# Kernel tuning notes

Measured on AMD Instinct MI355X. Metric: run time of the kernel, lower is better.

The kernel has to match this reference:

```python
import jax, jax.numpy as jnp
import numpy as np

K = 16  # number of nearest neighbors


def setup_inputs() -> dict:
    key = jax.random.key(0)
    k1, k2, k3 = jax.random.split(key, 3)
    B, N, C, C_OUT = 2, 8192, 64, 64
    coords_knn = jax.random.normal(k1, (B, N, 3), dtype=jnp.float32)
    feat = jax.random.normal(k2, (B, N, C), dtype=jnp.float32)
    # MLP params: Linear(2*C + 3 -> C_OUT)
    W = jax.random.normal(k3, (2 * C + 3, C_OUT), dtype=jnp.float32) * 0.05
    b = jnp.zeros((C_OUT,), dtype=jnp.float32)
    return {"coords_knn": coords_knn, "feat": feat, "W": W, "b": b}


def _knn_idx(coords, k):
    # pairwise squared distances: ||xi||^2 + ||xj||^2 - 2 xi.xj   -> [B, N, N]
    xx = jnp.sum(coords ** 2, axis=-1, keepdims=True)
    dist = xx + jnp.swapaxes(xx, 1, 2) - 2.0 * jnp.einsum('bnc,bmc->bnm', coords, coords)
    dist = jnp.maximum(dist, 0.0)
    _, idx = jax.lax.top_k(-dist, k)  # k smallest distances (order irrelevant: max-pool)
    return idx  # [B, N, k] int32


def reference(coords_knn, feat, W, b):
    idx = _knn_idx(coords_knn, K)
    gather = jax.vmap(lambda a, i: a[i])          # per-batch gather: [N,C],[N,k] -> [N,k,C]
    nb_f = gather(feat, idx)                      # [B, N, k, C]
    nb_p = gather(coords_knn, idx)                # [B, N, k, 3]
    fi = feat[:, :, None, :]                      # [B, N, 1, C]
    pi = coords_knn[:, :, None, :]                # [B, N, 1, 3]
    x = jnp.concatenate(
        [jnp.broadcast_to(fi, nb_f.shape), nb_f - fi, nb_p - pi], axis=-1
    )                                             # [B, N, k, 2C+3]
    x = jax.nn.relu(jnp.einsum('bnkd,do->bnko', x, W) + b)
    return jnp.max(x, axis=2)                     # [B, N, C_OUT]
```

## Files before the change

kernel.cpp:

```cpp
#include <hip/hip_runtime.h>
#include <hip/hip_bf16.h>
#include <stdint.h>
#include <float.h>

#define B_ 2
#define N_ 8192
#define C_ 64
#define K_ 16
#define D_IN 131
#define QPB 16
#define QPW 4
#define CAP 192
#define SAMPLE_N 2048

typedef __attribute__((ext_vector_type(8))) short short8v;
typedef __attribute__((ext_vector_type(4))) float f32x4;
typedef unsigned long long ull;

#define SENT_U64 0x7F7FFFFFFFFFFFFFull

__device__ __forceinline__ float sq3(float x, float y, float z) {
#pragma clang fp contract(off)
  return (x * x + y * y) + z * z;
}

__device__ __forceinline__ uint64_t shfl_xor_u64(uint64_t x, int mask) {
  int lo = __shfl_xor((int)(uint32_t)(x & 0xffffffffull), mask, 64);
  int hi = __shfl_xor((int)(uint32_t)(x >> 32), mask, 64);
  return ((uint64_t)(uint32_t)hi << 32) | (uint32_t)lo;
}

__device__ __forceinline__ double shfl_xor_f64(double x, int mask) {
  return __builtin_bit_cast(double, shfl_xor_u64(__builtin_bit_cast(uint64_t, x), mask));
}

__device__ __forceinline__ uint64_t pack_key_u64(float d, int idx) {
  return ((uint64_t)__float_as_uint(d) << 32) | (uint32_t)idx;
}

__device__ __forceinline__ short bfs(float x) {
  return __builtin_bit_cast(short, __float2bfloat16(x));
}

__device__ __forceinline__ void insert16(double* hd, double key) {
  hd[15] = key;
#pragma unroll
  for (int z = 15; z >= 1; --z) {
    double a = hd[z - 1], b = hd[z];
    hd[z - 1] = fmin(a, b);
    hd[z] = fmax(a, b);
  }
}

__device__ __forceinline__ float exact_d(float qx, float qy, float qz, float xxq,
                                         float4 cd) {
  float dot2 = fmaf(qz, cd.z, fmaf(qy, cd.y, qx * cd.x));
  float dtmp;
  {
#pragma clang fp contract(off)
    dtmp = (xxq + cd.w) - dot2;
  }
  return fmaxf(dtmp, 0.0f);
}

__global__ __launch_bounds__(256) void prep(const float* __restrict__ coords,
                                            const float* __restrict__ W,
                                            __hip_bfloat16* __restrict__ wfrag,
                                            float4* __restrict__ c4) {
  int i = blockIdx.x * 256 + threadIdx.x;
  if (i < 4 * 5 * 64 * 8) {
    int j = i & 7;
    int l = (i >> 3) & 63;
    int ks = (i >> 9) % 5;
    int nt = (i >> 9) / 5;
    int k = ks * 32 + (l >> 4) * 8 + j;
    int col = nt * 16 + (l & 15);
    float v = (k < D_IN) ? W[k * 64 + col] : 0.0f;
    wfrag[i] = __float2bfloat16(v);
  }
  int j2 = i - 4 * 5 * 64 * 8;
  if (j2 >= 0 && j2 < B_ * N_) {
    float cx = coords[j2 * 3 + 0], cy = coords[j2 * 3 + 1], cz = coords[j2 * 3 + 2];
    c4[j2] = make_float4(2.0f * cx, 2.0f * cy, 2.0f * cz, sq3(cx, cy, cz));
  }
}

__global__ __launch_bounds__(256) void knn_kernel(const float* __restrict__ coords,
                                                  const float4* __restrict__ c4,
                                                  int* __restrict__ idxout) {
  __shared__ int sbuf[QPB][CAP];
  __shared__ int scnt[QPB];
  const int t = threadIdx.x;
  const int w = t >> 6;
  const int lane = t & 63;
  const int blk = blockIdx.x;
  const int bb = blk >> 9;
  const int qbase = (blk & 511) * QPB;
  const float* cb = coords + (size_t)bb * N_ * 3;
  const float4* cg = c4 + (size_t)bb * N_;

  float qx[QPW], qy[QPW], qz[QPW], xxq[QPW];
#pragma unroll
  for (int r = 0; r < QPW; ++r) {
    int n = qbase + w * QPW + r;
    qx[r] = cb[n * 3 + 0]; qy[r] = cb[n * 3 + 1]; qz[r] = cb[n * 3 + 2];
    xxq[r] = sq3(qx[r], qy[r], qz[r]);
  }
  if (t < QPB) scnt[t] = 0;
  __syncthreads();

#define PROXY(r, cd) fmaf(qz[r], (cd).z, fmaf(qy[r], (cd).y, fmaf(qx[r], (cd).x, -(cd).w)))

  float M1[QPW], M2[QPW];
#pragma unroll
  for (int r = 0; r < QPW; ++r) { M1[r] = -FLT_MAX; M2[r] = -FLT_MAX; }

  for (int j0 = 0; j0 < SAMPLE_N; j0 += 512) {
    float4 c0 = cg[j0 + lane];
    float4 c1 = cg[j0 + 64 + lane];
    float4 c2 = cg[j0 + 128 + lane];
    float4 c3 = cg[j0 + 192 + lane];
    float4 c4v = cg[j0 + 256 + lane];
    float4 c5 = cg[j0 + 320 + lane];
    float4 c6 = cg[j0 + 384 + lane];
    float4 c7 = cg[j0 + 448 + lane];
#pragma unroll
    for (int r = 0; r < QPW; ++r) {
      float p0 = PROXY(r, c0);
      float p1 = PROXY(r, c1);
      float p2 = PROXY(r, c2);
      float p3 = PROXY(r, c3);
      float p4 = PROXY(r, c4v);
      float p5 = PROXY(r, c5);
      float p6 = PROXY(r, c6);
      float p7 = PROXY(r, c7);
      float a1 = fmaxf(p0, p1), b1 = fminf(p0, p1);
      float a2 = fmaxf(p2, p3), b2 = fminf(p2, p3);
      float a3 = fmaxf(p4, p5), b3 = fminf(p4, p5);
      float a4 = fmaxf(p6, p7), b4 = fminf(p6, p7);
      float h12 = fmaxf(a1, a2), s12 = fmaxf(fminf(a1, a2), fmaxf(b1, b2));
      float h34 = fmaxf(a3, a4), s34 = fmaxf(fminf(a3, a4), fmaxf(b3, b4));
      float hi = fmaxf(h12, h34);
      float se = fmaxf(fminf(h12, h34), fmaxf(s12, s34));
      float nm2 = fmaxf(fminf(M1[r], hi), fmaxf(M2[r], se));
      M1[r] = fmaxf(M1[r], hi);
      M2[r] = nm2;
    }
  }

  float A[QPW], Bt[QPW], pT[QPW];
#pragma unroll
  for (int r = 0; r < QPW; ++r) { A[r] = M1[r]; Bt[r] = M2[r]; pT[r] = -FLT_MAX; }
#pragma unroll
  for (int rd = 0; rd < 16; ++rd) {
#pragma unroll
    for (int r = 0; r < QPW; ++r) {
      float g = fmaxf(A[r], Bt[r]);
      g = fmaxf(g, __shfl_xor(g, 1, 64));
      g = fmaxf(g, __shfl_xor(g, 2, 64));
      g = fmaxf(g, __shfl_xor(g, 4, 64));
      g = fmaxf(g, __shfl_xor(g, 8, 64));
      g = fmaxf(g, __shfl_xor(g, 16, 64));
      g = fmaxf(g, __shfl_xor(g, 32, 64));
      pT[r] = g;
      A[r] = (A[r] == g) ? -FLT_MAX : A[r];
      Bt[r] = (Bt[r] == g) ? -FLT_MAX : Bt[r];
    }
  }
  float X[QPW];
#pragma unroll
  for (int r = 0; r < QPW; ++r) {
    float slop = 6e-6f * (fabsf(xxq[r]) + fabsf(pT[r])) + 1e-5f;
    X[r] = fminf(pT[r], xxq[r]) - 2.0f * slop;
  }

  for (int j0 = 0; j0 < N_; j0 += 512) {
    const int ia = j0 + lane;
    float4 c0 = cg[ia];
    float4 c1 = cg[ia + 64];
    float4 c2 = cg[ia + 128];
    float4 c3 = cg[ia + 192];
    float4 c4v = cg[ia + 256];
    float4 c5 = cg[ia + 320];
    float4 c6 = cg[ia + 384];
    float4 c7 = cg[ia + 448];
#pragma unroll
    for (int r = 0; r < QPW; ++r) {
      float p0 = PROXY(r, c0);
      float p1 = PROXY(r, c1);
      float p2 = PROXY(r, c2);
      float p3 = PROXY(r, c3);
      float p4 = PROXY(r, c4v);
      float p5 = PROXY(r, c5);
      float p6 = PROXY(r, c6);
      float p7 = PROXY(r, c7);
      const int qr = w * QPW + r;
      if (p0 >= X[r]) { int pos = atomicAdd(&scnt[qr], 1); if (pos < CAP) sbuf[qr][pos] = ia; }
      if (p1 >= X[r]) { int pos = atomicAdd(&scnt[qr], 1); if (pos < CAP) sbuf[qr][pos] = ia + 64; }
      if (p2 >= X[r]) { int pos = atomicAdd(&scnt[qr], 1); if (pos < CAP) sbuf[qr][pos] = ia + 128; }
      if (p3 >= X[r]) { int pos = atomicAdd(&scnt[qr], 1); if (pos < CAP) sbuf[qr][pos] = ia + 192; }
      if (p4 >= X[r]) { int pos = atomicAdd(&scnt[qr], 1); if (pos < CAP) sbuf[qr][pos] = ia + 256; }
      if (p5 >= X[r]) { int pos = atomicAdd(&scnt[qr], 1); if (pos < CAP) sbuf[qr][pos] = ia + 320; }
      if (p6 >= X[r]) { int pos = atomicAdd(&scnt[qr], 1); if (pos < CAP) sbuf[qr][pos] = ia + 384; }
      if (p7 >= X[r]) { int pos = atomicAdd(&scnt[qr], 1); if (pos < CAP) sbuf[qr][pos] = ia + 448; }
    }
  }
  __syncthreads();

  const int qloc = t >> 4;
  const int s16 = t & 15;
  const int n = qbase + qloc;

  const float fqx = cb[n * 3 + 0], fqy = cb[n * 3 + 1], fqz = cb[n * 3 + 2];
  const float fxx = sq3(fqx, fqy, fqz);

  double hd[16];
#pragma unroll
  for (int i = 0; i < 16; ++i) hd[i] = __builtin_bit_cast(double, SENT_U64);

  const int cntv = scnt[qloc];
  if (cntv > CAP) {
    for (int j = s16; j < N_; j += 16) {
      float cx = cb[j * 3 + 0], cy = cb[j * 3 + 1], cz = cb[j * 3 + 2];
      float ww = sq3(cx, cy, cz);
      float dot = fmaf(fqz, cz, fmaf(fqy, cy, fqx * cx));
      float d2;
      {
#pragma clang fp contract(off)
        d2 = (fxx + ww) - 2.0f * dot;
      }
      d2 = fmaxf(d2, 0.0f);
      double k = __builtin_bit_cast(double, pack_key_u64(d2, j));
      if (k < hd[15]) insert16(hd, k);
    }
  } else {
    for (int i = s16; i < cntv; i += 16) {
      int idx = sbuf[qloc][i];
      float d = exact_d(fqx, fqy, fqz, fxx, cg[idx]);
      double k = __builtin_bit_cast(double, pack_key_u64(d, idx));
      if (k < hd[15]) insert16(hd, k);
    }
  }

  int* myout = idxout + ((size_t)(bb * N_ + n)) * K_;
#pragma unroll
  for (int r = 0; r < 16; ++r) {
    double v = hd[0];
    v = fmin(v, shfl_xor_f64(v, 1));
    v = fmin(v, shfl_xor_f64(v, 2));
    v = fmin(v, shfl_xor_f64(v, 4));
    v = fmin(v, shfl_xor_f64(v, 8));
    if (__builtin_bit_cast(uint64_t, hd[0]) == __builtin_bit_cast(uint64_t, v)) {
#pragma unroll
      for (int z = 0; z < 15; ++z) hd[z] = hd[z + 1];
      hd[15] = __builtin_bit_cast(double, SENT_U64);
    }
    if (s16 == 0) myout[r] = (int)(uint32_t)__builtin_bit_cast(uint64_t, v);
  }
}

__global__ __launch_bounds__(256) void stage2(const float* __restrict__ coords,
                                              const float* __restrict__ feat,
                                              const int* __restrict__ idxbuf,
                                              const __hip_bfloat16* __restrict__ wfrag,
                                              const float* __restrict__ bias,
                                              float* __restrict__ out) {
  const int t = threadIdx.x;
  const int w = t >> 6;
  const int lane = t & 63;
  const int q = blockIdx.x * 4 + w;
  const int bb = q >> 13;
  const int n = q & (N_ - 1);
  const float* cb = coords + (size_t)bb * N_ * 3;
  const float* fb = feat + (size_t)bb * N_ * C_;
  const int* myidx = idxbuf + (size_t)q * K_;

  const int row = lane & 15;
  const int g = lane >> 4;
  const int nb = myidx[row];

  const float* fq = fb + (size_t)n * C_;
  const float* fn = fb + (size_t)nb * C_;

  float4 fi0 = *(const float4*)&fq[g * 8];
  float4 fi1 = *(const float4*)&fq[g * 8 + 4];
  float4 fi2 = *(const float4*)&fq[32 + g * 8];
  float4 fi3 = *(const float4*)&fq[32 + g * 8 + 4];
  float4 nf0 = *(const float4*)&fn[g * 8];
  float4 nf1 = *(const float4*)&fn[g * 8 + 4];
  float4 nf2 = *(const float4*)&fn[32 + g * 8];
  float4 nf3 = *(const float4*)&fn[32 + g * 8 + 4];

  short8v a[5];
  a[0] = (short8v){bfs(fi0.x), bfs(fi0.y), bfs(fi0.z), bfs(fi0.w),
                   bfs(fi1.x), bfs(fi1.y), bfs(fi1.z), bfs(fi1.w)};
  a[1] = (short8v){bfs(fi2.x), bfs(fi2.y), bfs(fi2.z), bfs(fi2.w),
                   bfs(fi3.x), bfs(fi3.y), bfs(fi3.z), bfs(fi3.w)};
  a[2] = (short8v){bfs(nf0.x - fi0.x), bfs(nf0.y - fi0.y), bfs(nf0.z - fi0.z), bfs(nf0.w - fi0.w),
                   bfs(nf1.x - fi1.x), bfs(nf1.y - fi1.y), bfs(nf1.z - fi1.z), bfs(nf1.w - fi1.w)};
  a[3] = (short8v){bfs(nf2.x - fi2.x), bfs(nf2.y - fi2.y), bfs(nf2.z - fi2.z), bfs(nf2.w - fi2.w),
                   bfs(nf3.x - fi3.x), bfs(nf3.y - fi3.y), bfs(nf3.z - fi3.z), bfs(nf3.w - fi3.w)};
  if (g == 0) {
    a[4] = (short8v){bfs(cb[nb * 3 + 0] - cb[n * 3 + 0]),
                     bfs(cb[nb * 3 + 1] - cb[n * 3 + 1]),
                     bfs(cb[nb * 3 + 2] - cb[n * 3 + 2]),
                     0, 0, 0, 0, 0};
  } else {
    a[4] = (short8v){0, 0, 0, 0, 0, 0, 0, 0};
  }

  const short8v* wf = (const short8v*)wfrag;
#pragma unroll
  for (int nt = 0; nt < 4; ++nt) {
    f32x4 acc = {0.f, 0.f, 0.f, 0.f};
#pragma unroll
    for (int ks = 0; ks < 5; ++ks) {
      short8v bf = wf[(nt * 5 + ks) * 64 + lane];
      acc = __builtin_amdgcn_mfma_f32_16x16x32_bf16(a[ks], bf, acc, 0, 0, 0);
    }
    float bcol = bias[nt * 16 + row];
    float m = fmaxf(fmaxf(fmaxf(acc[0] + bcol, 0.f), fmaxf(acc[1] + bcol, 0.f)),
                    fmaxf(fmaxf(acc[2] + bcol, 0.f), fmaxf(acc[3] + bcol, 0.f)));
    m = fmaxf(m, __shfl_xor(m, 16, 64));
    m = fmaxf(m, __shfl_xor(m, 32, 64));
    if (lane < 16) out[(size_t)q * C_ + nt * 16 + row] = m;
  }
}

extern "C" void kernel_launch(void* const* d_in, const int* in_sizes, int n_in,
                              void* d_out, int out_size, void* d_ws, size_t ws_size,
                              hipStream_t stream) {
  const float* coords = (const float*)d_in[0];
  const float* feat = (const float*)d_in[1];
  const float* W = (const float*)d_in[2];
  const float* bias = (const float*)d_in[3];
  float* out = (float*)d_out;

  int* ws_idx = (int*)d_ws;
  char* p = (char*)d_ws + (size_t)B_ * N_ * K_ * sizeof(int);
  __hip_bfloat16* wfrag = (__hip_bfloat16*)p;
  float4* c4 = (float4*)(p + 32768);

  const int prep_elems = 4 * 5 * 64 * 8 + B_ * N_;
  prep<<<(prep_elems + 255) / 256, 256, 0, stream>>>(coords, W, wfrag, c4);
  knn_kernel<<<(B_ * N_) / QPB, 256, 0, stream>>>(coords, c4, ws_idx);
  stage2<<<(B_ * N_) / 4, 256, 0, stream>>>(coords, feat, ws_idx, wfrag, bias, out);
}
```

Before: 91.13 us.

## Fuse KNN selection and MLP max-pool stage into one kernel

Merges the KNN kernel and the MFMA MLP stage into one kernel. Neighbor indices now stay in shared memory instead of going through a global workspace, and one kernel launch is removed. Each wave then runs the MLP for its 4 queries in sequence, so the MLP work is spread over far fewer blocks than the old stage2 grid. It also shares the KNN kernel's register and shared-memory footprint, which may lower occupancy for the gather and MFMA part.

```diff
diff --git a/kernel.cpp b/kernel.cpp
--- a/kernel.cpp
+++ b/kernel.cpp
@@ -85,11 +85,15 @@
   }
 }
 
-__global__ __launch_bounds__(256) void knn_kernel(const float* __restrict__ coords,
-                                                  const float4* __restrict__ c4,
-                                                  int* __restrict__ idxout) {
+__global__ __launch_bounds__(256) void knn_fused(const float* __restrict__ coords,
+                                                 const float4* __restrict__ c4,
+                                                 const float* __restrict__ feat,
+                                                 const __hip_bfloat16* __restrict__ wfrag,
+                                                 const float* __restrict__ bias,
+                                                 float* __restrict__ out) {
   __shared__ int sbuf[QPB][CAP];
   __shared__ int scnt[QPB];
+  __shared__ int sidx[QPB][K_];
   const int t = threadIdx.x;
   const int w = t >> 6;
   const int lane = t & 63;
@@ -242,7 +246,6 @@
     }
   }
 
-  int* myout = idxout + ((size_t)(bb * N_ + n)) * K_;
 #pragma unroll
   for (int r = 0; r < 16; ++r) {
     double v = hd[0];
@@ -255,75 +258,65 @@
       for (int z = 0; z < 15; ++z) hd[z] = hd[z + 1];
       hd[15] = __builtin_bit_cast(double, SENT_U64);
     }
-    if (s16 == 0) myout[r] = (int)(uint32_t)__builtin_bit_cast(uint64_t, v);
-  }
-}
-
-__global__ __launch_bounds__(256) void stage2(const float* __restrict__ coords,
-                                              const float* __restrict__ feat,
-                                              const int* __restrict__ idxbuf,
-                                              const __hip_bfloat16* __restrict__ wfrag,
-                                              const float* __restrict__ bias,
-                                              float* __restrict__ out) {
-  const int t = threadIdx.x;
-  const int w = t >> 6;
-  const int lane = t & 63;
-  const int q = blockIdx.x * 4 + w;
-  const int bb = q >> 13;
-  const int n = q & (N_ - 1);
-  const float* cb = coords + (size_t)bb * N_ * 3;
+    if (s16 == 0) sidx[qloc][r] = (int)(uint32_t)__builtin_bit_cast(uint64_t, v);
+  }
+  __syncthreads();
+
   const float* fb = feat + (size_t)bb * N_ * C_;
-  const int* myidx = idxbuf + (size_t)q * K_;
-
+  const short8v* wf = (const short8v*)wfrag;
   const int row = lane & 15;
   const int g = lane >> 4;
-  const int nb = myidx[row];
-
-  const float* fq = fb + (size_t)n * C_;
-  const float* fn = fb + (size_t)nb * C_;
-
-  float4 fi0 = *(const float4*)&fq[g * 8];
-  float4 fi1 = *(const float4*)&fq[g * 8 + 4];
-  float4 fi2 = *(const float4*)&fq[32 + g * 8];
-  float4 fi3 = *(const float4*)&fq[32 + g * 8 + 4];
-  float4 nf0 = *(const float4*)&fn[g * 8];
-  float4 nf1 = *(const float4*)&fn[g * 8 + 4];
-  float4 nf2 = *(const float4*)&fn[32 + g * 8];
-  float4 nf3 = *(const float4*)&fn[32 + g * 8 + 4];
-
-  short8v a[5];
-  a[0] = (short8v){bfs(fi0.x), bfs(fi0.y), bfs(fi0.z), bfs(fi0.w),
-                   bfs(fi1.x), bfs(fi1.y), bfs(fi1.z), bfs(fi1.w)};
-  a[1] = (short8v){bfs(fi2.x), bfs(fi2.y), bfs(fi2.z), bfs(fi2.w),
-                   bfs(fi3.x), bfs(fi3.y), bfs(fi3.z), bfs(fi3.w)};
-  a[2] = (short8v){bfs(nf0.x - fi0.x), bfs(nf0.y - fi0.y), bfs(nf0.z - fi0.z), bfs(nf0.w - fi0.w),
-                   bfs(nf1.x - fi1.x), bfs(nf1.y - fi1.y), bfs(nf1.z - fi1.z), bfs(nf1.w - fi1.w)};
-  a[3] = (short8v){bfs(nf2.x - fi2.x), bfs(nf2.y - fi2.y), bfs(nf2.z - fi2.z), bfs(nf2.w - fi2.w),
-                   bfs(nf3.x - fi3.x), bfs(nf3.y - fi3.y), bfs(nf3.z - fi3.z), bfs(nf3.w - fi3.w)};
-  if (g == 0) {
-    a[4] = (short8v){bfs(cb[nb * 3 + 0] - cb[n * 3 + 0]),
-                     bfs(cb[nb * 3 + 1] - cb[n * 3 + 1]),
-                     bfs(cb[nb * 3 + 2] - cb[n * 3 + 2]),
-                     0, 0, 0, 0, 0};
-  } else {
-    a[4] = (short8v){0, 0, 0, 0, 0, 0, 0, 0};
-  }
-
-  const short8v* wf = (const short8v*)wfrag;
-#pragma unroll
-  for (int nt = 0; nt < 4; ++nt) {
-    f32x4 acc = {0.f, 0.f, 0.f, 0.f};
-#pragma unroll
-    for (int ks = 0; ks < 5; ++ks) {
-      short8v bf = wf[(nt * 5 + ks) * 64 + lane];
-      acc = __builtin_amdgcn_mfma_f32_16x16x32_bf16(a[ks], bf, acc, 0, 0, 0);
-    }
-    float bcol = bias[nt * 16 + row];
-    float m = fmaxf(fmaxf(fmaxf(acc[0] + bcol, 0.f), fmaxf(acc[1] + bcol, 0.f)),
-                    fmaxf(fmaxf(acc[2] + bcol, 0.f), fmaxf(acc[3] + bcol, 0.f)));
-    m = fmaxf(m, __shfl_xor(m, 16, 64));
-    m = fmaxf(m, __shfl_xor(m, 32, 64));
-    if (lane < 16) out[(size_t)q * C_ + nt * 16 + row] = m;
+
+  for (int qi = 0; qi < QPW; ++qi) {
+    const int qloc2 = w * QPW + qi;
+    const int n2 = qbase + qloc2;
+    const int nb = sidx[qloc2][row];
+
+    const float* fq = fb + (size_t)n2 * C_;
+    const float* fn = fb + (size_t)nb * C_;
+
+    float4 fi0 = *(const float4*)&fq[g * 8];
+    float4 fi1 = *(const float4*)&fq[g * 8 + 4];
+    float4 fi2 = *(const float4*)&fq[32 + g * 8];
+    float4 fi3 = *(const float4*)&fq[32 + g * 8 + 4];
+    float4 nf0 = *(const float4*)&fn[g * 8];
+    float4 nf1 = *(const float4*)&fn[g * 8 + 4];
+    float4 nf2 = *(const float4*)&fn[32 + g * 8];
+    float4 nf3 = *(const float4*)&fn[32 + g * 8 + 4];
+
+    short8v a[5];
+    a[0] = (short8v){bfs(fi0.x), bfs(fi0.y), bfs(fi0.z), bfs(fi0.w),
+                     bfs(fi1.x), bfs(fi1.y), bfs(fi1.z), bfs(fi1.w)};
+    a[1] = (short8v){bfs(fi2.x), bfs(fi2.y), bfs(fi2.z), bfs(fi2.w),
+                     bfs(fi3.x), bfs(fi3.y), bfs(fi3.z), bfs(fi3.w)};
+    a[2] = (short8v){bfs(nf0.x - fi0.x), bfs(nf0.y - fi0.y), bfs(nf0.z - fi0.z), bfs(nf0.w - fi0.w),
+                     bfs(nf1.x - fi1.x), bfs(nf1.y - fi1.y), bfs(nf1.z - fi1.z), bfs(nf1.w - fi1.w)};
+    a[3] = (short8v){bfs(nf2.x - fi2.x), bfs(nf2.y - fi2.y), bfs(nf2.z - fi2.z), bfs(nf2.w - fi2.w),
+                     bfs(nf3.x - fi3.x), bfs(nf3.y - fi3.y), bfs(nf3.z - fi3.z), bfs(nf3.w - fi3.w)};
+    if (g == 0) {
+      a[4] = (short8v){bfs(cb[nb * 3 + 0] - cb[n2 * 3 + 0]),
+                       bfs(cb[nb * 3 + 1] - cb[n2 * 3 + 1]),
+                       bfs(cb[nb * 3 + 2] - cb[n2 * 3 + 2]),
+                       0, 0, 0, 0, 0};
+    } else {
+      a[4] = (short8v){0, 0, 0, 0, 0, 0, 0, 0};
+    }
+
+#pragma unroll
+    for (int nt = 0; nt < 4; ++nt) {
+      f32x4 acc = {0.f, 0.f, 0.f, 0.f};
+#pragma unroll
+      for (int ks = 0; ks < 5; ++ks) {
+        short8v bf = wf[(nt * 5 + ks) * 64 + lane];
+        acc = __builtin_amdgcn_mfma_f32_16x16x32_bf16(a[ks], bf, acc, 0, 0, 0);
+      }
+      float bcol = bias[nt * 16 + row];
+      float m = fmaxf(fmaxf(fmaxf(acc[0] + bcol, 0.f), fmaxf(acc[1] + bcol, 0.f)),
+                      fmaxf(fmaxf(acc[2] + bcol, 0.f), fmaxf(acc[3] + bcol, 0.f)));
+      m = fmaxf(m, __shfl_xor(m, 16, 64));
+      m = fmaxf(m, __shfl_xor(m, 32, 64));
+      if (lane < 16) out[(size_t)(bb * N_ + n2) * C_ + nt * 16 + row] = m;
+    }
   }
 }
 
@@ -336,13 +329,10 @@
   const float* bias = (const float*)d_in[3];
   float* out = (float*)d_out;
 
-  int* ws_idx = (int*)d_ws;
-  char* p = (char*)d_ws + (size_t)B_ * N_ * K_ * sizeof(int);
-  __hip_bfloat16* wfrag = (__hip_bfloat16*)p;
-  float4* c4 = (float4*)(p + 32768);
+  __hip_bfloat16* wfrag = (__hip_bfloat16*)d_ws;
+  float4* c4 = (float4*)((char*)d_ws + 32768);
 
   const int prep_elems = 4 * 5 * 64 * 8 + B_ * N_;
   prep<<<(prep_elems + 255) / 256, 256, 0, stream>>>(coords, W, wfrag, c4);
-  knn_kernel<<<(B_ * N_) / QPB, 256, 0, stream>>>(coords, c4, ws_idx);
-  stage2<<<(B_ * N_) / 4, 256, 0, stream>>>(coords, feat, ws_idx, wfrag, bias, out);
-}
+  knn_fused<<<(B_ * N_) / QPB, 256, 0, stream>>>(coords, c4, feat, wfrag, bias, out);
+}
```

After: 117.6 us. +29.0%, slower.
